# Kernel tuning notes

Measured on AMD Instinct MI355X. Metric: run time of the kernel, lower is better.

## Reference

```python
import jax, jax.numpy as jnp
import numpy as np

B, S, D, H = 4, 2048, 1024, 16
DK = D // H


def setup_inputs() -> dict:
    key = jax.random.key(0)
    ks = jax.random.split(key, 8)
    scale = 1.0 / np.sqrt(D)
    return {
        "q": jax.random.normal(ks[0], (B, S, D), jnp.float32),
        "k": jax.random.normal(ks[1], (B, S, D), jnp.float32),
        "v": jax.random.normal(ks[2], (B, S, D), jnp.float32),
        "mask": jnp.ones((1,), jnp.int32),  # unused (original code never applies it)
        "W_Q": jax.random.normal(ks[3], (D, D), jnp.float32) * scale,
        "W_K": jax.random.normal(ks[4], (D, D), jnp.float32) * scale,
        "W_V": jax.random.normal(ks[5], (D, D), jnp.float32) * scale,
        "W_O": jax.random.normal(ks[6], (D, D), jnp.float32) * scale,
    }


def reference(q, k, v, mask, W_Q, W_K, W_V, W_O):
    # nn.Linear(bias=False): y = x @ W.T ; weight shape [out, in]
    query = q @ W_Q.T  # [B,S,D]
    key_ = k @ W_K.T
    value = v @ W_V.T
    # split heads -> [B,H,S,DK]
    query = query.reshape(B, S, H, DK).transpose(0, 2, 1, 3)
    key_ = key_.reshape(B, S, H, DK).transpose(0, 2, 1, 3)
    value = value.reshape(B, S, H, DK).transpose(0, 2, 1, 3)
    # naive attention: full [B,H,S,S] score matrix (faithful to source)
    scores = jnp.einsum("bhqd,bhkd->bhqk", query, key_) / jnp.sqrt(
        jnp.asarray(DK, query.dtype)
    )
    attn = jax.nn.softmax(scores, axis=-1)  # dropout p=0.0 -> identity
    x = jnp.einsum("bhqk,bhkd->bhqd", attn, value)  # [B,H,S,DK]
    x = x.transpose(0, 2, 1, 3).reshape(B, S, D)
    return x @ W_O.T
```

## Files before the change

### kernel.cpp

```cpp
#include <hip/hip_runtime.h>
#include <math.h>


#define DEV __device__ __forceinline__

typedef __bf16 bf16x8 __attribute__((ext_vector_type(8)));
typedef float f32x4 __attribute__((ext_vector_type(4)));
typedef unsigned int u32x2 __attribute__((ext_vector_type(2)));

typedef __attribute__((address_space(1))) const unsigned int g_u32;
typedef __attribute__((address_space(3))) unsigned int l_u32;

DEV unsigned short f2bf(float x) {
  unsigned int u = __float_as_uint(x);
  u += 0x7fffu + ((u >> 16) & 1u);
  return (unsigned short)(u >> 16);
}

DEV unsigned int pack2bf(float a, float b) {
  return (unsigned int)f2bf(a) | ((unsigned int)f2bf(b) << 16);
}

DEV void ld16(const unsigned short* g, unsigned short* l) {
  __builtin_amdgcn_global_load_lds((g_u32*)g, (l_u32*)l, 16, 0, 0);
}

__global__ __launch_bounds__(256) void cast_f32_bf16(
    const float* __restrict__ src, unsigned short* __restrict__ dst, int n4) {
  int i = blockIdx.x * 256 + threadIdx.x;
  if (i < n4) {
    float4 v = reinterpret_cast<const float4*>(src)[i];
    ushort4 o;
    o.x = f2bf(v.x); o.y = f2bf(v.y); o.z = f2bf(v.z); o.w = f2bf(v.w);
    reinterpret_cast<ushort4*>(dst)[i] = o;
  }
}

DEV void gemm_core(const unsigned short* __restrict__ A,
                   const unsigned short* __restrict__ W,
                   unsigned short* As, unsigned short* Bs,
                   f32x4 (&acc)[4][4], int tileM, int tileN) {
  const int tid = threadIdx.x;
  const int w = tid >> 6, lane = tid & 63;
  const int wr = (w & 1) * 64, wc = (w >> 1) * 64;
  const int l15 = lane & 15, g4 = lane >> 4;
  const int srow = lane >> 2;
  const int scol = (lane & 3) * 8;

  const f32x4 fzero = {0.f, 0.f, 0.f, 0.f};
#pragma unroll
  for (int i = 0; i < 4; i++)
#pragma unroll
    for (int j = 0; j < 4; j++) acc[i][j] = fzero;

  for (int k0 = 0; k0 < 1024; k0 += 32) {
#pragma unroll
    for (int j = 0; j < 2; ++j) {
      int c = w * 2 + j;
      ld16(A + (size_t)(tileM + c * 16 + srow) * 1024 + k0 + scol, As + c * 512);
      ld16(W + (size_t)(tileN + c * 16 + srow) * 1024 + k0 + scol, Bs + c * 512);
    }
    __syncthreads();
    bf16x8 aF[4], bF[4];
#pragma unroll
    for (int i = 0; i < 4; i++)
      aF[i] = *reinterpret_cast<const bf16x8*>(&As[(wr + i * 16 + l15) * 32 + g4 * 8]);
#pragma unroll
    for (int j = 0; j < 4; j++)
      bF[j] = *reinterpret_cast<const bf16x8*>(&Bs[(wc + j * 16 + l15) * 32 + g4 * 8]);
#pragma unroll
    for (int i = 0; i < 4; i++)
#pragma unroll
      for (int j = 0; j < 4; j++)
        acc[i][j] = __builtin_amdgcn_mfma_f32_16x16x32_bf16(aF[i], bF[j], acc[i][j], 0, 0, 0);
    __syncthreads();
  }
}

__global__ __launch_bounds__(256) void gemm_qkv(
    const unsigned short* __restrict__ qb, const unsigned short* __restrict__ kb,
    const unsigned short* __restrict__ vb, const unsigned short* __restrict__ Wq,
    const unsigned short* __restrict__ Wk, const unsigned short* __restrict__ Wv,
    unsigned short* __restrict__ Qp, unsigned short* __restrict__ Kp,
    unsigned short* __restrict__ VpT) {
  __shared__ __align__(16) unsigned short As[128 * 32];
  __shared__ __align__(16) unsigned short Bs[128 * 32];
  const int z = blockIdx.z;
  const unsigned short* A = (z == 0) ? qb : (z == 1) ? kb : vb;
  const unsigned short* W = (z == 0) ? Wq : (z == 1) ? Wk : Wv;
  const int tileM = blockIdx.x * 128, tileN = blockIdx.y * 128;
  f32x4 acc[4][4];
  gemm_core(A, W, As, Bs, acc, tileM, tileN);

  const int tid = threadIdx.x, w = tid >> 6, lane = tid & 63;
  const int wr = (w & 1) * 64, wc = (w >> 1) * 64;
  const int l15 = lane & 15, g4 = lane >> 4;
  if (z < 2) {
    const float qs = (z == 0) ? 0.125f : 1.0f;
    unsigned short* C = (z == 0) ? Qp : Kp;
#pragma unroll
    for (int i = 0; i < 4; i++)
#pragma unroll
      for (int j = 0; j < 4; j++) {
        int col = tileN + wc + j * 16 + l15;
#pragma unroll
        for (int r = 0; r < 4; r++) {
          int row = tileM + wr + i * 16 + g4 * 4 + r;
          C[(size_t)row * 1024 + col] = f2bf(acc[i][j][r] * qs);
        }
      }
  } else {
    const int b = tileM / 2048, s0 = tileM % 2048;
#pragma unroll
    for (int i = 0; i < 4; i++)
#pragma unroll
      for (int j = 0; j < 4; j++) {
        int col = tileN + wc + j * 16 + l15;
        int s = s0 + wr + i * 16 + g4 * 4;
        ushort4 pk;
        pk.x = f2bf(acc[i][j][0]); pk.y = f2bf(acc[i][j][1]);
        pk.z = f2bf(acc[i][j][2]); pk.w = f2bf(acc[i][j][3]);
        *reinterpret_cast<ushort4*>(&VpT[(size_t)(b * 1024 + col) * 2048 + s]) = pk;
      }
  }
}

__global__ __launch_bounds__(256) void gemm_out(
    const unsigned short* __restrict__ Xp, const unsigned short* __restrict__ Wo,
    float* __restrict__ out) {
  __shared__ __align__(16) unsigned short As[128 * 32];
  __shared__ __align__(16) unsigned short Bs[128 * 32];
  const int tileM = blockIdx.x * 128, tileN = blockIdx.y * 128;
  f32x4 acc[4][4];
  gemm_core(Xp, Wo, As, Bs, acc, tileM, tileN);
  const int tid = threadIdx.x, w = tid >> 6, lane = tid & 63;
  const int wr = (w & 1) * 64, wc = (w >> 1) * 64;
  const int l15 = lane & 15, g4 = lane >> 4;
#pragma unroll
  for (int i = 0; i < 4; i++)
#pragma unroll
    for (int j = 0; j < 4; j++) {
      int col = tileN + wc + j * 16 + l15;
#pragma unroll
      for (int r = 0; r < 4; r++) {
        int row = tileM + wr + i * 16 + g4 * 4 + r;
        out[(size_t)row * 1024 + col] = acc[i][j][r];
      }
    }
}

__global__ __launch_bounds__(256, 4) void attn(
    const unsigned short* __restrict__ Qp, const unsigned short* __restrict__ Kp,
    const unsigned short* __restrict__ VpT, unsigned short* __restrict__ Xp) {
  __shared__ __align__(16) unsigned short Ks[64 * 64];
  __shared__ __align__(16) unsigned short Vs[64 * 64];
  __shared__ __align__(16) unsigned short Ps[4 * 32 * 64];

  const int bh = blockIdx.y, b = bh >> 4, h = bh & 15;
  const int q0 = blockIdx.x * 128;
  const int tid = threadIdx.x, w = tid >> 6, lane = tid & 63;
  const int l15 = lane & 15, g4 = lane >> 4;
  const int l7 = l15 & 7;

  const int rsub = lane >> 3;
  const int gsrc = (lane & 7) ^ rsub;

  bf16x8 qf[2][2];
#pragma unroll
  for (int mi = 0; mi < 2; mi++) {
    const unsigned short* Qrow =
        Qp + (size_t)(b * 2048 + q0 + w * 32 + mi * 16 + l15) * 1024 + h * 64;
    qf[mi][0] = *reinterpret_cast<const bf16x8*>(Qrow + g4 * 8);
    qf[mi][1] = *reinterpret_cast<const bf16x8*>(Qrow + 32 + g4 * 8);
  }

  const f32x4 fzero = {0.f, 0.f, 0.f, 0.f};
  f32x4 o[2][4];
#pragma unroll
  for (int mi = 0; mi < 2; mi++)
#pragma unroll
    for (int dj = 0; dj < 4; dj++) o[mi][dj] = fzero;
  float m_i[2] = {-INFINITY, -INFINITY};
  float l_i[2] = {0.f, 0.f};

  const unsigned short* Kbase = Kp + (size_t)(b * 2048) * 1024 + h * 64;
  const unsigned short* Vbase = VpT + (size_t)(b * 1024 + h * 64) * 2048;
  unsigned short* Pw = Ps + w * 2048;

  for (int kt = 0; kt < 2048; kt += 64) {
#pragma unroll
    for (int j = 0; j < 2; ++j) {
      int c = w * 2 + j;
      ld16(Kbase + (size_t)(kt + c * 8 + rsub) * 1024 + gsrc * 8, Ks + c * 512);
      ld16(Vbase + (size_t)(c * 8 + rsub) * 2048 + kt + gsrc * 8, Vs + c * 512);
    }
    __syncthreads();

    f32x4 sv[2][4];
#pragma unroll
    for (int jt = 0; jt < 4; jt++) {
      const int row = jt * 16 + l15;
      const int s0 = g4 ^ l7;
      bf16x8 kf0 = *reinterpret_cast<const bf16x8*>(&Ks[row * 64 + s0 * 8]);
      bf16x8 kf1 = *reinterpret_cast<const bf16x8*>(&Ks[row * 64 + (s0 ^ 4) * 8]);
#pragma unroll
      for (int mi = 0; mi < 2; mi++) {
        f32x4 z = fzero;
        z = __builtin_amdgcn_mfma_f32_16x16x32_bf16(kf0, qf[mi][0], z, 0, 0, 0);
        z = __builtin_amdgcn_mfma_f32_16x16x32_bf16(kf1, qf[mi][1], z, 0, 0, 0);
        sv[mi][jt] = z;
      }
    }

#pragma unroll
    for (int mi = 0; mi < 2; mi++) {
      float mx = sv[mi][0][0];
#pragma unroll
      for (int jt = 0; jt < 4; jt++)
#pragma unroll
        for (int r = 0; r < 4; r++) mx = fmaxf(mx, sv[mi][jt][r]);
      mx = fmaxf(mx, __shfl_xor(mx, 16));
      mx = fmaxf(mx, __shfl_xor(mx, 32));
      float mn = fmaxf(m_i[mi], mx);
      float al = __expf(m_i[mi] - mn);
      m_i[mi] = mn;
      float rs = 0.f;
#pragma unroll
      for (int jt = 0; jt < 4; jt++) {
#pragma unroll
        for (int r = 0; r < 4; r++) {
          sv[mi][jt][r] = __expf(sv[mi][jt][r] - mn);
          rs += sv[mi][jt][r];
        }
      }
      rs += __shfl_xor(rs, 16);
      rs += __shfl_xor(rs, 32);
      l_i[mi] = l_i[mi] * al + rs;
#pragma unroll
      for (int dj = 0; dj < 4; dj++) o[mi][dj] *= al;

      const int prow = mi * 16 + l15;
#pragma unroll
      for (int jt = 0; jt < 4; jt++) {
        u32x2 pk;
        pk.x = pack2bf(sv[mi][jt][0], sv[mi][jt][1]);
        pk.y = pack2bf(sv[mi][jt][2], sv[mi][jt][3]);
        const int slot = (jt * 4 + g4) ^ l15;
        *reinterpret_cast<u32x2*>(&Pw[prow * 64 + slot * 4]) = pk;
      }
    }

#pragma unroll
    for (int kc = 0; kc < 2; kc++) {
      bf16x8 vf[4];
#pragma unroll
      for (int dj = 0; dj < 4; dj++) {
        const int row = dj * 16 + l15;
        const int sg = (kc * 4 + g4) ^ l7;
        vf[dj] = *reinterpret_cast<const bf16x8*>(&Vs[row * 64 + sg * 8]);
      }
#pragma unroll
      for (int mi = 0; mi < 2; mi++) {
        const int prow = mi * 16 + l15;
        const int sA = (kc * 8 + g4 * 2) ^ l15;
        const int sB = (kc * 8 + g4 * 2 + 1) ^ l15;
        u32x2 pa = *reinterpret_cast<const u32x2*>(&Pw[prow * 64 + sA * 4]);
        u32x2 pb = *reinterpret_cast<const u32x2*>(&Pw[prow * 64 + sB * 4]);
        union { unsigned int u[4]; bf16x8 v; } pf;
        pf.u[0] = pa.x; pf.u[1] = pa.y; pf.u[2] = pb.x; pf.u[3] = pb.y;
#pragma unroll
        for (int dj = 0; dj < 4; dj++)
          o[mi][dj] = __builtin_amdgcn_mfma_f32_16x16x32_bf16(vf[dj], pf.v, o[mi][dj], 0, 0, 0);
      }
    }
    __syncthreads();
  }

#pragma unroll
  for (int mi = 0; mi < 2; mi++) {
    const float inv = 1.f / l_i[mi];
    const size_t row = (size_t)(b * 2048 + q0 + w * 32 + mi * 16 + l15);
#pragma unroll
    for (int dj = 0; dj < 4; dj++) {
      ushort4 pk;
      pk.x = f2bf(o[mi][dj][0] * inv);
      pk.y = f2bf(o[mi][dj][1] * inv);
      pk.z = f2bf(o[mi][dj][2] * inv);
      pk.w = f2bf(o[mi][dj][3] * inv);
      *reinterpret_cast<ushort4*>(&Xp[row * 1024 + h * 64 + dj * 16 + g4 * 4]) = pk;
    }
  }
}

extern "C" void kernel_launch(void* const* d_in, const int* in_sizes, int n_in,
                              void* d_out, int out_size, void* d_ws, size_t ws_size,
                              hipStream_t stream) {
  const float* q  = (const float*)d_in[0];
  const float* k  = (const float*)d_in[1];
  const float* v  = (const float*)d_in[2];
  const float* Wq = (const float*)d_in[4];
  const float* Wk = (const float*)d_in[5];
  const float* Wv = (const float*)d_in[6];
  const float* Wo = (const float*)d_in[7];
  float* out = (float*)d_out;

  char* ws = (char*)d_ws;
  const size_t MB = 1u << 20;
  unsigned short* qb  = (unsigned short*)(ws + 0 * MB);
  unsigned short* kb  = (unsigned short*)(ws + 16 * MB);
  unsigned short* vb  = (unsigned short*)(ws + 32 * MB);
  unsigned short* wqb = (unsigned short*)(ws + 48 * MB);
  unsigned short* wkb = (unsigned short*)(ws + 50 * MB);
  unsigned short* wvb = (unsigned short*)(ws + 52 * MB);
  unsigned short* wob = (unsigned short*)(ws + 54 * MB);
  unsigned short* Qp  = (unsigned short*)(ws + 56 * MB);
  unsigned short* Kp  = (unsigned short*)(ws + 72 * MB);
  unsigned short* VpT = (unsigned short*)(ws + 88 * MB);
  unsigned short* Xp  = (unsigned short*)(ws + 104 * MB);

  const int n4_t = (4 * 2048 * 1024) / 4;
  const int n4_w = (1024 * 1024) / 4;
  cast_f32_bf16<<<n4_t / 256, 256, 0, stream>>>(q, qb, n4_t);
  cast_f32_bf16<<<n4_t / 256, 256, 0, stream>>>(k, kb, n4_t);
  cast_f32_bf16<<<n4_t / 256, 256, 0, stream>>>(v, vb, n4_t);
  cast_f32_bf16<<<n4_w / 256, 256, 0, stream>>>(Wq, wqb, n4_w);
  cast_f32_bf16<<<n4_w / 256, 256, 0, stream>>>(Wk, wkb, n4_w);
  cast_f32_bf16<<<n4_w / 256, 256, 0, stream>>>(Wv, wvb, n4_w);
  cast_f32_bf16<<<n4_w / 256, 256, 0, stream>>>(Wo, wob, n4_w);

  dim3 gq(64, 8, 3);
  gemm_qkv<<<gq, 256, 0, stream>>>(qb, kb, vb, wqb, wkb, wvb, Qp, Kp, VpT);

  dim3 ga(16, 64);
  attn<<<ga, 256, 0, stream>>>(Qp, Kp, VpT, Xp);

  dim3 go(64, 8, 1);
  gemm_out<<<go, 256, 0, stream>>>(Xp, wob, out);
}
```

Baseline: 428.7 us.

## Double-buffer K/V tiles, use exp2 softmax, merge cast launches

Attention now double-buffers the K and V tiles in LDS, prefetching the next tile while the current one is computed, which removes one barrier per iteration. Softmax uses exp2 with log2(e) folded into the Q scale, and P packing uses a cheaper round-half-up bf16 conversion. The P scratch is shrunk to 16 rows per wave and reused across mi, and V fragments are loaded inline. Seven cast launches are merged into two. Risks: more LDS per block, a slightly different rounding of P, and a possible race on the shared P buffer being reused between mi iterations within a wave.

```diff
diff --git a/kernel.cpp b/kernel.cpp
--- a/kernel.cpp
+++ b/kernel.cpp
@@ -18,22 +18,50 @@
 }
 
 DEV unsigned int pack2bf(float a, float b) {
-  return (unsigned int)f2bf(a) | ((unsigned int)f2bf(b) << 16);
+  unsigned int ua = __float_as_uint(a) + 0x8000u;
+  unsigned int ub = __float_as_uint(b) + 0x8000u;
+  return (ua >> 16) | (ub & 0xffff0000u);
+}
+
+DEV float fexp2(float x) {
+#if __has_builtin(__builtin_amdgcn_exp2f)
+  return __builtin_amdgcn_exp2f(x);
+#else
+  return __expf(x * 0.69314718056f);
+#endif
 }
 
 DEV void ld16(const unsigned short* g, unsigned short* l) {
   __builtin_amdgcn_global_load_lds((g_u32*)g, (l_u32*)l, 16, 0, 0);
 }
 
-__global__ __launch_bounds__(256) void cast_f32_bf16(
-    const float* __restrict__ src, unsigned short* __restrict__ dst, int n4) {
+__global__ __launch_bounds__(256) void cast_qkv(
+    const float* __restrict__ q, const float* __restrict__ k,
+    const float* __restrict__ v, unsigned short* __restrict__ qb,
+    unsigned short* __restrict__ kb, unsigned short* __restrict__ vb) {
+  const int z = blockIdx.y;
+  const float* src = (z == 0) ? q : (z == 1) ? k : v;
+  unsigned short* dst = (z == 0) ? qb : (z == 1) ? kb : vb;
   int i = blockIdx.x * 256 + threadIdx.x;
-  if (i < n4) {
-    float4 v = reinterpret_cast<const float4*>(src)[i];
-    ushort4 o;
-    o.x = f2bf(v.x); o.y = f2bf(v.y); o.z = f2bf(v.z); o.w = f2bf(v.w);
-    reinterpret_cast<ushort4*>(dst)[i] = o;
-  }
+  float4 vv = reinterpret_cast<const float4*>(src)[i];
+  ushort4 o;
+  o.x = f2bf(vv.x); o.y = f2bf(vv.y); o.z = f2bf(vv.z); o.w = f2bf(vv.w);
+  reinterpret_cast<ushort4*>(dst)[i] = o;
+}
+
+__global__ __launch_bounds__(256) void cast_w(
+    const float* __restrict__ w0, const float* __restrict__ w1,
+    const float* __restrict__ w2, const float* __restrict__ w3,
+    unsigned short* __restrict__ o0, unsigned short* __restrict__ o1,
+    unsigned short* __restrict__ o2, unsigned short* __restrict__ o3) {
+  const int z = blockIdx.y;
+  const float* src = (z == 0) ? w0 : (z == 1) ? w1 : (z == 2) ? w2 : w3;
+  unsigned short* dst = (z == 0) ? o0 : (z == 1) ? o1 : (z == 2) ? o2 : o3;
+  int i = blockIdx.x * 256 + threadIdx.x;
+  float4 vv = reinterpret_cast<const float4*>(src)[i];
+  ushort4 o;
+  o.x = f2bf(vv.x); o.y = f2bf(vv.y); o.z = f2bf(vv.z); o.w = f2bf(vv.w);
+  reinterpret_cast<ushort4*>(dst)[i] = o;
 }
 
 DEV void gemm_core(const unsigned short* __restrict__ A,
@@ -96,7 +124,7 @@
   const int wr = (w & 1) * 64, wc = (w >> 1) * 64;
   const int l15 = lane & 15, g4 = lane >> 4;
   if (z < 2) {
-    const float qs = (z == 0) ? 0.125f : 1.0f;
+    const float qs = (z == 0) ? 0.125f * 1.44269504089f : 1.0f;
     unsigned short* C = (z == 0) ? Qp : Kp;
 #pragma unroll
     for (int i = 0; i < 4; i++)
@@ -152,9 +180,9 @@
 __global__ __launch_bounds__(256, 4) void attn(
     const unsigned short* __restrict__ Qp, const unsigned short* __restrict__ Kp,
     const unsigned short* __restrict__ VpT, unsigned short* __restrict__ Xp) {
-  __shared__ __align__(16) unsigned short Ks[64 * 64];
-  __shared__ __align__(16) unsigned short Vs[64 * 64];
-  __shared__ __align__(16) unsigned short Ps[4 * 32 * 64];
+  __shared__ __align__(16) unsigned short Ks[2][64 * 64];
+  __shared__ __align__(16) unsigned short Vs[2][64 * 64];
+  __shared__ __align__(16) unsigned short Ps[4 * 16 * 64];
 
   const int bh = blockIdx.y, b = bh >> 4, h = bh & 15;
   const int q0 = blockIdx.x * 128;
@@ -185,24 +213,39 @@
 
   const unsigned short* Kbase = Kp + (size_t)(b * 2048) * 1024 + h * 64;
   const unsigned short* Vbase = VpT + (size_t)(b * 1024 + h * 64) * 2048;
-  unsigned short* Pw = Ps + w * 2048;
-
+  unsigned short* Pw = Ps + w * 1024;
+
+#pragma unroll
+  for (int j = 0; j < 2; ++j) {
+    const int c = w * 2 + j;
+    ld16(Kbase + (size_t)(c * 8 + rsub) * 1024 + gsrc * 8, &Ks[0][c * 512]);
+    ld16(Vbase + (size_t)(c * 8 + rsub) * 2048 + gsrc * 8, &Vs[0][c * 512]);
+  }
+
+#pragma unroll 2
   for (int kt = 0; kt < 2048; kt += 64) {
-#pragma unroll
-    for (int j = 0; j < 2; ++j) {
-      int c = w * 2 + j;
-      ld16(Kbase + (size_t)(kt + c * 8 + rsub) * 1024 + gsrc * 8, Ks + c * 512);
-      ld16(Vbase + (size_t)(c * 8 + rsub) * 2048 + kt + gsrc * 8, Vs + c * 512);
-    }
+    const int cur = (kt >> 6) & 1;
     __syncthreads();
+    if (kt + 64 < 2048) {
+#pragma unroll
+      for (int j = 0; j < 2; ++j) {
+        const int c = w * 2 + j;
+        ld16(Kbase + (size_t)(kt + 64 + c * 8 + rsub) * 1024 + gsrc * 8,
+             &Ks[cur ^ 1][c * 512]);
+        ld16(Vbase + (size_t)(c * 8 + rsub) * 2048 + (kt + 64) + gsrc * 8,
+             &Vs[cur ^ 1][c * 512]);
+      }
+    }
+    const unsigned short* Kc = Ks[cur];
+    const unsigned short* Vc = Vs[cur];
 
     f32x4 sv[2][4];
 #pragma unroll
     for (int jt = 0; jt < 4; jt++) {
       const int row = jt * 16 + l15;
       const int s0 = g4 ^ l7;
-      bf16x8 kf0 = *reinterpret_cast<const bf16x8*>(&Ks[row * 64 + s0 * 8]);
-      bf16x8 kf1 = *reinterpret_cast<const bf16x8*>(&Ks[row * 64 + (s0 ^ 4) * 8]);
+      bf16x8 kf0 = *reinterpret_cast<const bf16x8*>(&Kc[row * 64 + s0 * 8]);
+      bf16x8 kf1 = *reinterpret_cast<const bf16x8*>(&Kc[row * 64 + (s0 ^ 4) * 8]);
 #pragma unroll
       for (int mi = 0; mi < 2; mi++) {
         f32x4 z = fzero;
@@ -222,58 +265,47 @@
       mx = fmaxf(mx, __shfl_xor(mx, 16));
       mx = fmaxf(mx, __shfl_xor(mx, 32));
       float mn = fmaxf(m_i[mi], mx);
-      float al = __expf(m_i[mi] - mn);
+      float al = fexp2(m_i[mi] - mn);
       m_i[mi] = mn;
       float rs = 0.f;
 #pragma unroll
-      for (int jt = 0; jt < 4; jt++) {
+      for (int jt = 0; jt < 4; jt++)
 #pragma unroll
         for (int r = 0; r < 4; r++) {
-          sv[mi][jt][r] = __expf(sv[mi][jt][r] - mn);
+          sv[mi][jt][r] = fexp2(sv[mi][jt][r] - mn);
           rs += sv[mi][jt][r];
         }
-      }
       rs += __shfl_xor(rs, 16);
       rs += __shfl_xor(rs, 32);
       l_i[mi] = l_i[mi] * al + rs;
 #pragma unroll
       for (int dj = 0; dj < 4; dj++) o[mi][dj] *= al;
 
-      const int prow = mi * 16 + l15;
 #pragma unroll
       for (int jt = 0; jt < 4; jt++) {
         u32x2 pk;
         pk.x = pack2bf(sv[mi][jt][0], sv[mi][jt][1]);
         pk.y = pack2bf(sv[mi][jt][2], sv[mi][jt][3]);
         const int slot = (jt * 4 + g4) ^ l15;
-        *reinterpret_cast<u32x2*>(&Pw[prow * 64 + slot * 4]) = pk;
-      }
-    }
-
-#pragma unroll
-    for (int kc = 0; kc < 2; kc++) {
-      bf16x8 vf[4];
-#pragma unroll
-      for (int dj = 0; dj < 4; dj++) {
-        const int row = dj * 16 + l15;
-        const int sg = (kc * 4 + g4) ^ l7;
-        vf[dj] = *reinterpret_cast<const bf16x8*>(&Vs[row * 64 + sg * 8]);
-      }
-#pragma unroll
-      for (int mi = 0; mi < 2; mi++) {
-        const int prow = mi * 16 + l15;
+        *reinterpret_cast<u32x2*>(&Pw[l15 * 64 + slot * 4]) = pk;
+      }
+
+#pragma unroll
+      for (int kc = 0; kc < 2; kc++) {
         const int sA = (kc * 8 + g4 * 2) ^ l15;
         const int sB = (kc * 8 + g4 * 2 + 1) ^ l15;
-        u32x2 pa = *reinterpret_cast<const u32x2*>(&Pw[prow * 64 + sA * 4]);
-        u32x2 pb = *reinterpret_cast<const u32x2*>(&Pw[prow * 64 + sB * 4]);
+        u32x2 pa = *reinterpret_cast<const u32x2*>(&Pw[l15 * 64 + sA * 4]);
+        u32x2 pb = *reinterpret_cast<const u32x2*>(&Pw[l15 * 64 + sB * 4]);
         union { unsigned int u[4]; bf16x8 v; } pf;
         pf.u[0] = pa.x; pf.u[1] = pa.y; pf.u[2] = pb.x; pf.u[3] = pb.y;
 #pragma unroll
-        for (int dj = 0; dj < 4; dj++)
-          o[mi][dj] = __builtin_amdgcn_mfma_f32_16x16x32_bf16(vf[dj], pf.v, o[mi][dj], 0, 0, 0);
-      }
-    }
-    __syncthreads();
+        for (int dj = 0; dj < 4; dj++) {
+          bf16x8 vf = *reinterpret_cast<const bf16x8*>(
+              &Vc[(dj * 16 + l15) * 64 + ((kc * 4 + g4) ^ l7) * 8]);
+          o[mi][dj] = __builtin_amdgcn_mfma_f32_16x16x32_bf16(vf, pf.v, o[mi][dj], 0, 0, 0);
+        }
+      }
+    }
   }
 
 #pragma unroll
@@ -318,15 +350,10 @@
   unsigned short* VpT = (unsigned short*)(ws + 88 * MB);
   unsigned short* Xp  = (unsigned short*)(ws + 104 * MB);
 
-  const int n4_t = (4 * 2048 * 1024) / 4;
-  const int n4_w = (1024 * 1024) / 4;
-  cast_f32_bf16<<<n4_t / 256, 256, 0, stream>>>(q, qb, n4_t);
-  cast_f32_bf16<<<n4_t / 256, 256, 0, stream>>>(k, kb, n4_t);
-  cast_f32_bf16<<<n4_t / 256, 256, 0, stream>>>(v, vb, n4_t);
-  cast_f32_bf16<<<n4_w / 256, 256, 0, stream>>>(Wq, wqb, n4_w);
-  cast_f32_bf16<<<n4_w / 256, 256, 0, stream>>>(Wk, wkb, n4_w);
-  cast_f32_bf16<<<n4_w / 256, 256, 0, stream>>>(Wv, wvb, n4_w);
-  cast_f32_bf16<<<n4_w / 256, 256, 0, stream>>>(Wo, wob, n4_w);
+  dim3 gc(8192, 3);
+  cast_qkv<<<gc, 256, 0, stream>>>(q, k, v, qb, kb, vb);
+  dim3 gw(1024, 4);
+  cast_w<<<gw, 256, 0, stream>>>(Wq, Wk, Wv, Wo, wqb, wkb, wvb, wob);
 
   dim3 gq(64, 8, 3);
   gemm_qkv<<<gq, 256, 0, stream>>>(qb, kb, vb, wqb, wkb, wvb, Qp, Kp, VpT);
```

New measurement: 484.1 us. +12.9%, slower.
